# Kernel optimization log

Hardware: AMD Instinct MI355X
Metric: run time of the kernel (lower is better)

The kernel has to match this reference:

```python
import jax, jax.numpy as jnp
import numpy as np

EPS = 1e-8

def setup_inputs() -> dict:
    key = jax.random.key(0)
    k1, k2, k3 = jax.random.split(key, 3)
    central_value = jax.random.normal(k1, (256, 512), dtype=jnp.float32)
    partial_deviations = jax.random.normal(k2, (256, 256, 512), dtype=jnp.float32)
    err = jax.random.uniform(k3, (256, 512), dtype=jnp.float32)
    return {"central_value": central_value, "partial_deviations": partial_deviations, "err": err}


def reference(central_value, partial_deviations, err):
    # calculate_range: zonotope interval bounds
    radius = jnp.sum(jnp.abs(partial_deviations), axis=1) + jnp.abs(err)  # (B, D)
    lower = central_value - radius
    upper = central_value + radius

    rl = jax.nn.relu(lower)
    ru = jax.nn.relu(upper)
    lam = (ru - rl) / (upper - lower + EPS)
    lam = jnp.where(lower >= 0, 1.0, lam)
    lam = jnp.where(upper < 0, 0.0, lam)
    lam = jnp.nan_to_num(lam, nan=0.0)
    lam = jnp.clip(lam, 0.0, 1.0)
    beta = (rl - lam * lower) * 0.5
    delta = jnp.abs(beta)

    # apply_linear_approx
    new_central = lam * central_value + beta                              # (B, D)
    scaled_pd = partial_deviations * lam[:, None, :]                      # (B, N, D)
    d = central_value.shape[-1]
    diag = delta[:, :, None] * jnp.eye(d, dtype=delta.dtype)              # diag_embed -> (B, D, D)
    new_pd = jnp.concatenate([scaled_pd, diag], axis=1)                   # (B, N+D, D)
    new_err = lam * err
    return (new_central, new_pd, new_err)
```

## Files before the change

### kernel.cpp

```cpp
#include <hip/hip_runtime.h>

#define BB 256
#define NN 256
#define DD 512
#define RT (NN + DD)
#define D4 (DD / 4)

constexpr float EPSF = 1e-8f;
constexpr size_t PD_OFF = (size_t)BB * DD;
constexpr size_t NE_OFF = PD_OFF + (size_t)BB * RT * DD;

typedef float vfloat4 __attribute__((ext_vector_type(4)));


__device__ __forceinline__ vfloat4 nt_load4(const vfloat4* p) {
    return __builtin_nontemporal_load(p);
}
__device__ __forceinline__ void nt_store4(vfloat4* p, vfloat4 v) {
    __builtin_nontemporal_store(v, p);
}

__device__ __forceinline__ void relax1(float rad, float c,
                                       float& l, float& beta) {
    const float lo = c - rad, up = c + rad;
    const float rl = fmaxf(lo, 0.f), ru = fmaxf(up, 0.f);
    l = (ru - rl) / (up - lo + EPSF);
    if (lo >= 0.f) l = 1.f;
    if (up <  0.f) l = 0.f;
    if (l != l)    l = 0.f;
    l = fminf(fmaxf(l, 0.f), 1.f);
    beta = (rl - l * lo) * 0.5f;
}

__global__ __launch_bounds__(1024) void reduce_kernel(
    const float* __restrict__ cv, const float* __restrict__ pd,
    const float* __restrict__ err, float* __restrict__ out)
{
    const int b   = blockIdx.x;
    const int tid = threadIdx.x;
    const int d4  = tid & (D4 - 1);
    const int rg  = tid >> 7;

    const vfloat4* pdb = (const vfloat4*)pd + (size_t)b * NN * D4;
    float ax = 0.f, ay = 0.f, az = 0.f, aw = 0.f;
#pragma unroll 8
    for (int it = 0; it < NN / 8; ++it) {
        vfloat4 v = nt_load4(pdb + (size_t)((it << 3) + rg) * D4 + d4);
        ax += fabsf(v.x); ay += fabsf(v.y); az += fabsf(v.z); aw += fabsf(v.w);
    }

    __shared__ vfloat4 part[8][D4];
    {
        vfloat4 s;
        s.x = ax; s.y = ay; s.z = az; s.w = aw;
        part[rg][d4] = s;
    }
    __syncthreads();

    if (tid < D4) {
        vfloat4 rad = part[0][tid];
#pragma unroll
        for (int g = 1; g < 8; ++g) {
            vfloat4 p = part[g][tid];
            rad.x += p.x; rad.y += p.y; rad.z += p.z; rad.w += p.w;
        }
        const size_t gi4 = (size_t)b * D4 + tid;
        const vfloat4 c = ((const vfloat4*)cv)[gi4];
        const vfloat4 e = ((const vfloat4*)err)[gi4];
        vfloat4 l4, b4;
        float l, beta;
        relax1(rad.x + fabsf(e.x), c.x, l, beta);  l4.x = l; b4.x = beta;
        relax1(rad.y + fabsf(e.y), c.y, l, beta);  l4.y = l; b4.y = beta;
        relax1(rad.z + fabsf(e.z), c.z, l, beta);  l4.z = l; b4.z = beta;
        relax1(rad.w + fabsf(e.w), c.w, l, beta);  l4.w = l; b4.w = beta;
        ((vfloat4*)(out + NE_OFF))[gi4] = l4;
        ((vfloat4*)out)[gi4]            = b4;
    }
}

#define WBLOCKS 2048
#define RPB (BB * RT / WBLOCKS)

__global__ __launch_bounds__(256) void pd_kernel(
    const float* __restrict__ pd, float* out )
{
    const int bx  = blockIdx.x;
    const int b   = bx >> 3;
    const int tid = threadIdx.x;
    const int d4  = tid & (D4 - 1);
    const int ro  = tid >> 7;

    const vfloat4 lm  = ((const vfloat4*)(out + NE_OFF))[(size_t)b * D4 + d4];
    const float*  bet = out + (size_t)b * DD;
    const vfloat4* pdb  = (const vfloat4*)pd + (size_t)b * NN * D4;
    vfloat4*       outb = (vfloat4*)(out + PD_OFF) + (size_t)b * RT * D4;

    int r = (bx & 7) * RPB + ro;
#pragma unroll 4
    for (int i = 0; i < RPB / 2; ++i, r += 2) {
        vfloat4 v;
        if (r < NN) {
            vfloat4 pv = nt_load4(pdb + (size_t)r * D4 + d4);
            v.x = pv.x * lm.x; v.y = pv.y * lm.y;
            v.z = pv.z * lm.z; v.w = pv.w * lm.w;
        } else {
            const int dg = r - NN;
            v.x = 0.f; v.y = 0.f; v.z = 0.f; v.w = 0.f;
            if (d4 == (dg >> 2))
                v[dg & 3] = fabsf(bet[dg]);
        }
        nt_store4(outb + (size_t)r * D4 + d4, v);
    }
}

__global__ __launch_bounds__(256) void finalize_kernel(
    const float* __restrict__ cv, const float* __restrict__ err,
    float* out )
{
    const size_t i = (size_t)blockIdx.x * 256 + threadIdx.x;
    const vfloat4 l  = ((const vfloat4*)(out + NE_OFF))[i];
    const vfloat4 bt = ((const vfloat4*)out)[i];
    const vfloat4 c  = ((const vfloat4*)cv)[i];
    const vfloat4 e  = ((const vfloat4*)err)[i];
    vfloat4 nc, ne;
    nc.x = l.x * c.x + bt.x;  ne.x = l.x * e.x;
    nc.y = l.y * c.y + bt.y;  ne.y = l.y * e.y;
    nc.z = l.z * c.z + bt.z;  ne.z = l.z * e.z;
    nc.w = l.w * c.w + bt.w;  ne.w = l.w * e.w;
    ((vfloat4*)out)[i]            = nc;
    ((vfloat4*)(out + NE_OFF))[i] = ne;
}

extern "C" void kernel_launch(void* const* d_in, const int* in_sizes, int n_in,
                              void* d_out, int out_size, void* d_ws, size_t ws_size,
                              hipStream_t stream) {
    const float* cv  = (const float*)d_in[0];
    const float* pd  = (const float*)d_in[1];
    const float* err = (const float*)d_in[2];
    float* out = (float*)d_out;

    reduce_kernel<<<dim3(BB), dim3(1024), 0, stream>>>(cv, pd, err, out);
    pd_kernel<<<dim3(WBLOCKS), dim3(256), 0, stream>>>(pd, out);
    finalize_kernel<<<dim3(BB * DD / 4 / 256), dim3(256), 0, stream>>>(cv, err, out);
}
```

Measured before the change: 549.7 us.

## Split pd kernel into scale and zero-fill blocks, write diagonal in finalize

Splits pd_kernel into two block roles. One set of blocks scales the partial-deviation rows, the other fills the diagonal region with zeros using pure streaming stores, with no per-element branch or beta lookup. The diagonal values are then scattered in finalize_kernel, which now runs one block per batch. Loads from the input deviations switch from nontemporal to normal cached loads, so the second read in pd_kernel can hit in cache after reduce_kernel. This adds a scattered write pass over the diagonal and relies on stream ordering to put it after the zero fill.

```diff
diff --git a/kernel.cpp b/kernel.cpp
--- a/kernel.cpp
+++ b/kernel.cpp
@@ -13,9 +13,6 @@
 typedef float vfloat4 __attribute__((ext_vector_type(4)));
 
 
-__device__ __forceinline__ vfloat4 nt_load4(const vfloat4* p) {
-    return __builtin_nontemporal_load(p);
-}
 __device__ __forceinline__ void nt_store4(vfloat4* p, vfloat4 v) {
     __builtin_nontemporal_store(v, p);
 }
@@ -45,7 +42,7 @@
     float ax = 0.f, ay = 0.f, az = 0.f, aw = 0.f;
 #pragma unroll 8
     for (int it = 0; it < NN / 8; ++it) {
-        vfloat4 v = nt_load4(pdb + (size_t)((it << 3) + rg) * D4 + d4);
+        vfloat4 v = pdb[(size_t)((it << 3) + rg) * D4 + d4];
         ax += fabsf(v.x); ay += fabsf(v.y); az += fabsf(v.z); aw += fabsf(v.w);
     }
 
@@ -78,38 +75,39 @@
     }
 }
 
-#define WBLOCKS 2048
-#define RPB (BB * RT / WBLOCKS)
-
 __global__ __launch_bounds__(256) void pd_kernel(
     const float* __restrict__ pd, float* out )
 {
     const int bx  = blockIdx.x;
-    const int b   = bx >> 3;
     const int tid = threadIdx.x;
-    const int d4  = tid & (D4 - 1);
-    const int ro  = tid >> 7;
 
-    const vfloat4 lm  = ((const vfloat4*)(out + NE_OFF))[(size_t)b * D4 + d4];
-    const float*  bet = out + (size_t)b * DD;
-    const vfloat4* pdb  = (const vfloat4*)pd + (size_t)b * NN * D4;
-    vfloat4*       outb = (vfloat4*)(out + PD_OFF) + (size_t)b * RT * D4;
+    if (bx < 2048) {
+        const int b  = bx >> 3;
+        const int d4 = tid & (D4 - 1);
+        const int ro = tid >> 7;
+        const vfloat4 lm = ((const vfloat4*)(out + NE_OFF))[(size_t)b * D4 + d4];
+        const vfloat4* pdb  = (const vfloat4*)pd + (size_t)b * NN * D4;
+        vfloat4*       outb = (vfloat4*)(out + PD_OFF) + (size_t)b * RT * D4;
 
-    int r = (bx & 7) * RPB + ro;
+        int r = (bx & 7) * 32 + ro;
 #pragma unroll 4
-    for (int i = 0; i < RPB / 2; ++i, r += 2) {
-        vfloat4 v;
-        if (r < NN) {
-            vfloat4 pv = nt_load4(pdb + (size_t)r * D4 + d4);
+        for (int i = 0; i < 16; ++i, r += 2) {
+            vfloat4 pv = pdb[(size_t)r * D4 + d4];
+            vfloat4 v;
             v.x = pv.x * lm.x; v.y = pv.y * lm.y;
             v.z = pv.z * lm.z; v.w = pv.w * lm.w;
-        } else {
-            const int dg = r - NN;
-            v.x = 0.f; v.y = 0.f; v.z = 0.f; v.w = 0.f;
-            if (d4 == (dg >> 2))
-                v[dg & 3] = fabsf(bet[dg]);
+            nt_store4(outb + (size_t)r * D4 + d4, v);
         }
-        nt_store4(outb + (size_t)r * D4 + d4, v);
+    } else {
+        const int zb = bx - 2048;
+        const int b  = zb >> 3;
+        vfloat4* base = (vfloat4*)(out + PD_OFF) + (size_t)b * RT * D4
+                      + (size_t)NN * D4 + (size_t)(zb & 7) * 8192;
+        vfloat4 z;
+        z.x = 0.f; z.y = 0.f; z.z = 0.f; z.w = 0.f;
+#pragma unroll 8
+        for (int it = 0; it < 32; ++it)
+            nt_store4(base + it * 256 + tid, z);
     }
 }
 
@@ -117,18 +115,32 @@
     const float* __restrict__ cv, const float* __restrict__ err,
     float* out )
 {
-    const size_t i = (size_t)blockIdx.x * 256 + threadIdx.x;
-    const vfloat4 l  = ((const vfloat4*)(out + NE_OFF))[i];
-    const vfloat4 bt = ((const vfloat4*)out)[i];
-    const vfloat4 c  = ((const vfloat4*)cv)[i];
-    const vfloat4 e  = ((const vfloat4*)err)[i];
-    vfloat4 nc, ne;
-    nc.x = l.x * c.x + bt.x;  ne.x = l.x * e.x;
-    nc.y = l.y * c.y + bt.y;  ne.y = l.y * e.y;
-    nc.z = l.z * c.z + bt.z;  ne.z = l.z * e.z;
-    nc.w = l.w * c.w + bt.w;  ne.w = l.w * e.w;
-    ((vfloat4*)out)[i]            = nc;
-    ((vfloat4*)(out + NE_OFF))[i] = ne;
+    const int b   = blockIdx.x;
+    const int tid = threadIdx.x;
+    const float* bet = out + (size_t)b * DD;
+
+    const float b0 = bet[tid];
+    const float b1 = bet[tid + 256];
+    float* diag = out + PD_OFF + (size_t)b * RT * DD + (size_t)NN * DD;
+    diag[(size_t)tid * DD + tid]                 = fabsf(b0);
+    diag[(size_t)(tid + 256) * DD + (tid + 256)] = fabsf(b1);
+
+    __syncthreads();
+
+    if (tid < D4) {
+        const size_t gi4 = (size_t)b * D4 + tid;
+        const vfloat4 l  = ((const vfloat4*)(out + NE_OFF))[gi4];
+        const vfloat4 bt = ((const vfloat4*)out)[gi4];
+        const vfloat4 c  = ((const vfloat4*)cv)[gi4];
+        const vfloat4 e  = ((const vfloat4*)err)[gi4];
+        vfloat4 nc, ne;
+        nc.x = l.x * c.x + bt.x;  ne.x = l.x * e.x;
+        nc.y = l.y * c.y + bt.y;  ne.y = l.y * e.y;
+        nc.z = l.z * c.z + bt.z;  ne.z = l.z * e.z;
+        nc.w = l.w * c.w + bt.w;  ne.w = l.w * e.w;
+        ((vfloat4*)out)[gi4]            = nc;
+        ((vfloat4*)(out + NE_OFF))[gi4] = ne;
+    }
 }
 
 extern "C" void kernel_launch(void* const* d_in, const int* in_sizes, int n_in,
@@ -140,6 +152,6 @@
     float* out = (float*)d_out;
 
     reduce_kernel<<<dim3(BB), dim3(1024), 0, stream>>>(cv, pd, err, out);
-    pd_kernel<<<dim3(WBLOCKS), dim3(256), 0, stream>>>(pd, out);
-    finalize_kernel<<<dim3(BB * DD / 4 / 256), dim3(256), 0, stream>>>(cv, err, out);
+    pd_kernel<<<dim3(4096), dim3(256), 0, stream>>>(pd, out);
+    finalize_kernel<<<dim3(BB), dim3(256), 0, stream>>>(cv, err, out);
 }
```

Measured after the change: 514.4 us. 6.4% less time.
